# Performance work log

Hardware: AMD Instinct MI355X
Metric: run time of the kernel (lower is better)

The kernel has to match this reference:

```python
import jax, jax.numpy as jnp
import numpy as np

NUM_LAYERS = 2
IN_DIM = 256
OUT_DIM = 256
N = 8192


def setup_inputs() -> dict:
    key = jax.random.key(0)
    k = jax.random.split(key, 7)
    x = jax.random.normal(k[0], (N, IN_DIM), dtype=jnp.float32)
    adj = jax.random.uniform(k[1], (N, N), dtype=jnp.float32)
    # MLP params (Linear: y = x @ W.T + b); kaiming-ish scale
    W1 = jax.random.normal(k[2], (OUT_DIM, IN_DIM), dtype=jnp.float32) / np.sqrt(IN_DIM)
    b1 = jnp.zeros((OUT_DIM,), dtype=jnp.float32)
    W2 = jax.random.normal(k[3], (OUT_DIM, OUT_DIM), dtype=jnp.float32) / np.sqrt(OUT_DIM)
    b2 = jnp.zeros((OUT_DIM,), dtype=jnp.float32)
    epsilon = jnp.zeros((1,), dtype=jnp.float32)  # torch init: Tensor([0.0])
    return {"x": x, "adj": adj, "W1": W1, "b1": b1, "W2": W2, "b2": b2, "epsilon": epsilon}


def reference(x, adj, W1, b1, W2, b2, epsilon):
    for _ in range(NUM_LAYERS):
        # epsilon-weighted neighborhood aggregation + residual
        x = x + epsilon * (adj @ x)          # [N, d]
        # 2-layer MLP (shared across layers, as in the torch module)
        h = jax.nn.relu(x @ W1.T + b1)       # [N, out]
        x = h @ W2.T + b2                    # [N, out]
    return x
```

## Files before the change

### kernel.cpp

```cpp
#include <hip/hip_runtime.h>
#include <hip/hip_bf16.h>

typedef __hip_bfloat16 bf16;
typedef short s16x8 __attribute__((ext_vector_type(8)));
typedef float f32x4 __attribute__((ext_vector_type(4)));

static constexpr int NROWS = 8192;
static constexpr int DIM   = 256;

__device__ inline float to_f(float v) { return v; }
__device__ inline float to_f(bf16 v)  { return __bfloat162float(v); }
__device__ inline unsigned short f2bf(float f) {
    bf16 h = __float2bfloat16(f);
    return __builtin_bit_cast(unsigned short, h);
}

__global__ void convW_kernel(const float* __restrict__ W1, const float* __restrict__ W2,
                             bf16* __restrict__ W1b, bf16* __restrict__ W2b) {
    const int b = blockIdx.x;
    const float* src = (b < 64) ? W1 : W2;
    bf16*       dst = (b < 64) ? W1b : W2b;
    const int t = (b & 63) * 256 + threadIdx.x;
    float4 v = ((const float4*)src)[t];
    ((ushort4*)dst)[t] = make_ushort4(f2bf(v.x), f2bf(v.y), f2bf(v.z), f2bf(v.w));
}

template<typename TIN, bool OUTF32>
__global__ __launch_bounds__(256, 1)
void fused_mlp(const TIN* __restrict__ A, const float* __restrict__ adj,
               const float* __restrict__ eps_p,
               const bf16* __restrict__ W1, const float* __restrict__ b1,
               const bf16* __restrict__ W2, const float* __restrict__ b2,
               void* __restrict__ C) {
    constexpr int K = 256;
    constexpr int PITCH = 264;
    __shared__ short Xs[32][PITCH];
    __shared__ short Hs[32][PITCH];

    const int tid  = threadIdx.x;
    const int lane = tid & 63;
    const int wave = tid >> 6;
    const int lr = lane & 15;
    const int q  = lane >> 4;
    const int row0 = blockIdx.x * 32;
    const float eps = *eps_p;

    if (eps == 0.0f) {
#pragma unroll
        for (int p = 0; p < 4; ++p) {
            const int id = p * 256 + tid;
            const int r  = id >> 5;
            const int c  = (id & 31) * 8;
            if constexpr (sizeof(TIN) == 4) {
                const float* src = (const float*)A + (size_t)(row0 + r) * K + c;
                float4 v0 = *(const float4*)(src);
                float4 v1 = *(const float4*)(src + 4);
                *(ushort4*)(&Xs[r][c])     = make_ushort4(f2bf(v0.x), f2bf(v0.y), f2bf(v0.z), f2bf(v0.w));
                *(ushort4*)(&Xs[r][c + 4]) = make_ushort4(f2bf(v1.x), f2bf(v1.y), f2bf(v1.z), f2bf(v1.w));
            } else {
                *(uint4*)(&Xs[r][c]) = *(const uint4*)((const bf16*)A + (size_t)(row0 + r) * K + c);
            }
        }
    } else {
        for (int r = 0; r < 32; ++r) {
            const int row = row0 + r;
            float s = 0.0f;
            const float* arow = adj + (size_t)row * NROWS;
            for (int k = 0; k < NROWS; ++k)
                s += arow[k] * to_f(A[(size_t)k * DIM + tid]);
            Xs[r][tid] = (short)f2bf(to_f(A[(size_t)row * DIM + tid]) + eps * s);
        }
    }
    __syncthreads();

    f32x4 acc1[4][2] = {};
    const bf16* W1p = W1 + (size_t)(wave * 64 + lr) * K + q * 8;
#pragma unroll
    for (int kk = 0; kk < 8; ++kk) {
        s16x8 wf[4], xf[2];
#pragma unroll
        for (int i = 0; i < 4; ++i)
            wf[i] = *(const s16x8*)(W1p + (size_t)i * 16 * K + kk * 32);
#pragma unroll
        for (int j = 0; j < 2; ++j)
            xf[j] = *(const s16x8*)(&Xs[j * 16 + lr][kk * 32 + q * 8]);
#pragma unroll
        for (int i = 0; i < 4; ++i)
#pragma unroll
            for (int j = 0; j < 2; ++j)
                acc1[i][j] = __builtin_amdgcn_mfma_f32_16x16x32_bf16(
                    wf[i], xf[j], acc1[i][j], 0, 0, 0);
    }

#pragma unroll
    for (int i = 0; i < 4; ++i) {
        const int hc = wave * 64 + i * 16 + q * 4;
        const float4 bv = *(const float4*)(b1 + hc);
#pragma unroll
        for (int j = 0; j < 2; ++j) {
            ushort4 hv;
            hv.x = f2bf(fmaxf(acc1[i][j][0] + bv.x, 0.0f));
            hv.y = f2bf(fmaxf(acc1[i][j][1] + bv.y, 0.0f));
            hv.z = f2bf(fmaxf(acc1[i][j][2] + bv.z, 0.0f));
            hv.w = f2bf(fmaxf(acc1[i][j][3] + bv.w, 0.0f));
            *(ushort4*)(&Hs[j * 16 + lr][hc]) = hv;
        }
    }
    __syncthreads();

    f32x4 acc2[2][4] = {};
    const bf16* W2p = W2 + (size_t)(wave * 64 + lr) * K + q * 8;
#pragma unroll
    for (int kk = 0; kk < 8; ++kk) {
        s16x8 hf[2], wf[4];
#pragma unroll
        for (int j = 0; j < 4; ++j)
            wf[j] = *(const s16x8*)(W2p + (size_t)j * 16 * K + kk * 32);
#pragma unroll
        for (int i = 0; i < 2; ++i)
            hf[i] = *(const s16x8*)(&Hs[i * 16 + lr][kk * 32 + q * 8]);
#pragma unroll
        for (int i = 0; i < 2; ++i)
#pragma unroll
            for (int j = 0; j < 4; ++j)
                acc2[i][j] = __builtin_amdgcn_mfma_f32_16x16x32_bf16(
                    hf[i], wf[j], acc2[i][j], 0, 0, 0);
    }

#pragma unroll
    for (int i = 0; i < 2; ++i) {
#pragma unroll
        for (int j = 0; j < 4; ++j) {
            const int col = wave * 64 + j * 16 + lr;
            const float bv = b2[col];
#pragma unroll
            for (int r = 0; r < 4; ++r) {
                const int row = row0 + i * 16 + q * 4 + r;
                float v = acc2[i][j][r] + bv;
                if (OUTF32) ((float*)C)[(size_t)row * DIM + col] = v;
                else        ((bf16*)C)[(size_t)row * DIM + col] = __float2bfloat16(v);
            }
        }
    }
}

extern "C" void kernel_launch(void* const* d_in, const int* in_sizes, int n_in,
                              void* d_out, int out_size, void* d_ws, size_t ws_size,
                              hipStream_t stream) {
    const float* x   = (const float*)d_in[0];
    const float* adj = (const float*)d_in[1];
    const float* W1  = (const float*)d_in[2];
    const float* b1  = (const float*)d_in[3];
    const float* W2  = (const float*)d_in[4];
    const float* b2  = (const float*)d_in[5];
    const float* eps = (const float*)d_in[6];
    float* out = (float*)d_out;

    char* ws = (char*)d_ws;
    bf16* W1b   = (bf16*)ws;  ws += (size_t)DIM * DIM * 2;
    bf16* W2b   = (bf16*)ws;  ws += (size_t)DIM * DIM * 2;
    bf16* bufY1 = (bf16*)ws;  ws += (size_t)NROWS * DIM * 2;

    convW_kernel<<<128, 256, 0, stream>>>(W1, W2, W1b, W2b);
    fused_mlp<float, false><<<NROWS / 32, 256, 0, stream>>>(x, adj, eps, W1b, b1, W2b, b2, bufY1);
    fused_mlp<bf16,  true ><<<NROWS / 32, 256, 0, stream>>>(bufY1, adj, eps, W1b, b1, W2b, b2, out);
}
```

Measured before the change: 331.9 us.

## Fuse both GIN layers into one kernel with register-resident weight fragments

When epsilon is zero, the two MLP layers now run in a single kernel. The intermediate activations stay in LDS instead of going out to a bf16 global buffer, which removes a kernel launch and a full global round trip. W1 and W2 fragments are loaded into registers once per block and reused across all four GEMM phases, and the output stores are widened to float4. The nonzero-epsilon path moves to separate fallback kernels that exit early, so the default path still pays for two extra empty launches and carries more register pressure from holding 64 weight fragments per thread.

```diff
diff --git a/kernel.cpp b/kernel.cpp
--- a/kernel.cpp
+++ b/kernel.cpp
@@ -7,6 +7,8 @@
 
 static constexpr int NROWS = 8192;
 static constexpr int DIM   = 256;
+static constexpr int KDIM  = 256;
+static constexpr int PITCH = 264;
 
 __device__ inline float to_f(float v) { return v; }
 __device__ inline float to_f(bf16 v)  { return __bfloat162float(v); }
@@ -15,25 +17,133 @@
     return __builtin_bit_cast(unsigned short, h);
 }
 
-__global__ void convW_kernel(const float* __restrict__ W1, const float* __restrict__ W2,
-                             bf16* __restrict__ W1b, bf16* __restrict__ W2b) {
-    const int b = blockIdx.x;
-    const float* src = (b < 64) ? W1 : W2;
-    bf16*       dst = (b < 64) ? W1b : W2b;
-    const int t = (b & 63) * 256 + threadIdx.x;
-    float4 v = ((const float4*)src)[t];
-    ((ushort4*)dst)[t] = make_ushort4(f2bf(v.x), f2bf(v.y), f2bf(v.z), f2bf(v.w));
-}
-
-template<typename TIN, bool OUTF32>
+__global__ void agg0_convW_kernel(const float* __restrict__ x, const float* __restrict__ adj,
+                                  const float* __restrict__ W1, const float* __restrict__ W2,
+                                  const float* __restrict__ eps_p,
+                                  bf16* __restrict__ W1b, bf16* __restrict__ W2b,
+                                  float* __restrict__ y) {
+    {
+        const int b = blockIdx.x;
+        const float* src = (b < 64) ? W1 : W2;
+        bf16*       dst = (b < 64) ? W1b : W2b;
+        const int t = (b & 63) * 256 + threadIdx.x;
+        float4 v = ((const float4*)src)[t];
+        ((ushort4*)dst)[t] = make_ushort4(f2bf(v.x), f2bf(v.y), f2bf(v.z), f2bf(v.w));
+    }
+    const float eps = *eps_p;
+    if (eps == 0.0f) return;
+    const size_t total = (size_t)NROWS * DIM;
+    for (size_t e = (size_t)blockIdx.x * blockDim.x + threadIdx.x;
+         e < total;
+         e += (size_t)gridDim.x * blockDim.x) {
+        const int i = (int)(e >> 8);
+        const int j = (int)(e & 255);
+        float s = 0.0f;
+        const float* arow = adj + (size_t)i * NROWS;
+        for (int k = 0; k < NROWS; ++k)
+            s += arow[k] * x[(size_t)k * DIM + j];
+        y[e] = x[e] + eps * s;
+    }
+}
+
+template<bool RELU>
+__device__ __forceinline__ void mlp_phase_lds(const s16x8 (&wf)[8][4],
+                                              short (*src)[PITCH], short (*dst)[PITCH],
+                                              const float* __restrict__ bias,
+                                              int wave, int lr, int q) {
+    f32x4 acc[4][2] = {};
+#pragma unroll
+    for (int kk = 0; kk < 8; ++kk) {
+        s16x8 xf[2];
+#pragma unroll
+        for (int j = 0; j < 2; ++j)
+            xf[j] = *(const s16x8*)(&src[j * 16 + lr][kk * 32 + q * 8]);
+#pragma unroll
+        for (int i = 0; i < 4; ++i)
+#pragma unroll
+            for (int j = 0; j < 2; ++j)
+                acc[i][j] = __builtin_amdgcn_mfma_f32_16x16x32_bf16(
+                    wf[kk][i], xf[j], acc[i][j], 0, 0, 0);
+    }
+#pragma unroll
+    for (int i = 0; i < 4; ++i) {
+        const int oc = wave * 64 + i * 16 + q * 4;
+        const float4 bv = *(const float4*)(bias + oc);
+#pragma unroll
+        for (int j = 0; j < 2; ++j) {
+            float v0 = acc[i][j][0] + bv.x;
+            float v1 = acc[i][j][1] + bv.y;
+            float v2 = acc[i][j][2] + bv.z;
+            float v3 = acc[i][j][3] + bv.w;
+            if (RELU) {
+                v0 = fmaxf(v0, 0.0f); v1 = fmaxf(v1, 0.0f);
+                v2 = fmaxf(v2, 0.0f); v3 = fmaxf(v3, 0.0f);
+            }
+            *(ushort4*)(&dst[j * 16 + lr][oc]) =
+                make_ushort4(f2bf(v0), f2bf(v1), f2bf(v2), f2bf(v3));
+        }
+    }
+}
+
+template<bool OUTF32>
+__device__ __forceinline__ void mlp_phase_out(const s16x8 (&wf)[8][4],
+                                              short (*src)[PITCH],
+                                              const float* __restrict__ bias,
+                                              void* __restrict__ C,
+                                              int wave, int lr, int q, int row0) {
+    f32x4 acc[4][2] = {};
+#pragma unroll
+    for (int kk = 0; kk < 8; ++kk) {
+        s16x8 xf[2];
+#pragma unroll
+        for (int j = 0; j < 2; ++j)
+            xf[j] = *(const s16x8*)(&src[j * 16 + lr][kk * 32 + q * 8]);
+#pragma unroll
+        for (int i = 0; i < 4; ++i)
+#pragma unroll
+            for (int j = 0; j < 2; ++j)
+                acc[i][j] = __builtin_amdgcn_mfma_f32_16x16x32_bf16(
+                    wf[kk][i], xf[j], acc[i][j], 0, 0, 0);
+    }
+#pragma unroll
+    for (int i = 0; i < 4; ++i) {
+        const int oc = wave * 64 + i * 16 + q * 4;
+        const float4 bv = *(const float4*)(bias + oc);
+#pragma unroll
+        for (int j = 0; j < 2; ++j) {
+            const int row = row0 + j * 16 + lr;
+            float v0 = acc[i][j][0] + bv.x;
+            float v1 = acc[i][j][1] + bv.y;
+            float v2 = acc[i][j][2] + bv.z;
+            float v3 = acc[i][j][3] + bv.w;
+            if (OUTF32) {
+                float4 o; o.x = v0; o.y = v1; o.z = v2; o.w = v3;
+                *(float4*)(&((float*)C)[(size_t)row * DIM + oc]) = o;
+            } else {
+                *(ushort4*)(&((bf16*)C)[(size_t)row * DIM + oc]) =
+                    make_ushort4(f2bf(v0), f2bf(v1), f2bf(v2), f2bf(v3));
+            }
+        }
+    }
+}
+
+__device__ __forceinline__ void load_wfrags(const bf16* __restrict__ W,
+                                            s16x8 (&wf)[8][4],
+                                            int wave, int lr, int q) {
+    const bf16* Wp = W + (size_t)(wave * 64 + lr) * KDIM + q * 8;
+#pragma unroll
+    for (int kk = 0; kk < 8; ++kk)
+#pragma unroll
+        for (int i = 0; i < 4; ++i)
+            wf[kk][i] = *(const s16x8*)(Wp + (size_t)i * 16 * KDIM + kk * 32);
+}
+
 __global__ __launch_bounds__(256, 1)
-void fused_mlp(const TIN* __restrict__ A, const float* __restrict__ adj,
-               const float* __restrict__ eps_p,
-               const bf16* __restrict__ W1, const float* __restrict__ b1,
-               const bf16* __restrict__ W2, const float* __restrict__ b2,
-               void* __restrict__ C) {
-    constexpr int K = 256;
-    constexpr int PITCH = 264;
+void mega_gin(const float* __restrict__ x, const float* __restrict__ eps_p,
+              const bf16* __restrict__ W1, const float* __restrict__ b1,
+              const bf16* __restrict__ W2, const float* __restrict__ b2,
+              float* __restrict__ out) {
+    if (*eps_p != 0.0f) return;
     __shared__ short Xs[32][PITCH];
     __shared__ short Hs[32][PITCH];
 
@@ -43,25 +153,57 @@
     const int lr = lane & 15;
     const int q  = lane >> 4;
     const int row0 = blockIdx.x * 32;
+
+    s16x8 w1f[8][4], w2f[8][4];
+    load_wfrags(W1, w1f, wave, lr, q);
+    load_wfrags(W2, w2f, wave, lr, q);
+
+#pragma unroll
+    for (int p = 0; p < 4; ++p) {
+        const int id = p * 256 + tid;
+        const int r  = id >> 5;
+        const int c  = (id & 31) * 8;
+        const float* src = x + (size_t)(row0 + r) * KDIM + c;
+        float4 v0 = *(const float4*)(src);
+        float4 v1 = *(const float4*)(src + 4);
+        *(ushort4*)(&Xs[r][c])     = make_ushort4(f2bf(v0.x), f2bf(v0.y), f2bf(v0.z), f2bf(v0.w));
+        *(ushort4*)(&Xs[r][c + 4]) = make_ushort4(f2bf(v1.x), f2bf(v1.y), f2bf(v1.z), f2bf(v1.w));
+    }
+    __syncthreads();
+
+    mlp_phase_lds<true >(w1f, Xs, Hs, b1, wave, lr, q);
+    __syncthreads();
+    mlp_phase_lds<false>(w2f, Hs, Xs, b2, wave, lr, q);
+    __syncthreads();
+    mlp_phase_lds<true >(w1f, Xs, Hs, b1, wave, lr, q);
+    __syncthreads();
+    mlp_phase_out<true >(w2f, Hs, b2, out, wave, lr, q, row0);
+}
+
+template<typename TIN, bool OUTF32, bool DO_AGG>
+__global__ __launch_bounds__(256, 1)
+void fb_mlp(const TIN* __restrict__ A, const float* __restrict__ adj,
+            const float* __restrict__ eps_p,
+            const bf16* __restrict__ W1, const float* __restrict__ b1,
+            const bf16* __restrict__ W2, const float* __restrict__ b2,
+            void* __restrict__ C) {
     const float eps = *eps_p;
-
-    if (eps == 0.0f) {
-#pragma unroll
-        for (int p = 0; p < 4; ++p) {
-            const int id = p * 256 + tid;
-            const int r  = id >> 5;
-            const int c  = (id & 31) * 8;
-            if constexpr (sizeof(TIN) == 4) {
-                const float* src = (const float*)A + (size_t)(row0 + r) * K + c;
-                float4 v0 = *(const float4*)(src);
-                float4 v1 = *(const float4*)(src + 4);
-                *(ushort4*)(&Xs[r][c])     = make_ushort4(f2bf(v0.x), f2bf(v0.y), f2bf(v0.z), f2bf(v0.w));
-                *(ushort4*)(&Xs[r][c + 4]) = make_ushort4(f2bf(v1.x), f2bf(v1.y), f2bf(v1.z), f2bf(v1.w));
-            } else {
-                *(uint4*)(&Xs[r][c]) = *(const uint4*)((const bf16*)A + (size_t)(row0 + r) * K + c);
-            }
-        }
-    } else {
+    if (eps == 0.0f) return;
+    __shared__ short Xs[32][PITCH];
+    __shared__ short Hs[32][PITCH];
+
+    const int tid  = threadIdx.x;
+    const int lane = tid & 63;
+    const int wave = tid >> 6;
+    const int lr = lane & 15;
+    const int q  = lane >> 4;
+    const int row0 = blockIdx.x * 32;
+
+    s16x8 w1f[8][4], w2f[8][4];
+    load_wfrags(W1, w1f, wave, lr, q);
+    load_wfrags(W2, w2f, wave, lr, q);
+
+    if (DO_AGG) {
         for (int r = 0; r < 32; ++r) {
             const int row = row0 + r;
             float s = 0.0f;
@@ -70,78 +212,28 @@
                 s += arow[k] * to_f(A[(size_t)k * DIM + tid]);
             Xs[r][tid] = (short)f2bf(to_f(A[(size_t)row * DIM + tid]) + eps * s);
         }
-    }
-    __syncthreads();
-
-    f32x4 acc1[4][2] = {};
-    const bf16* W1p = W1 + (size_t)(wave * 64 + lr) * K + q * 8;
-#pragma unroll
-    for (int kk = 0; kk < 8; ++kk) {
-        s16x8 wf[4], xf[2];
-#pragma unroll
-        for (int i = 0; i < 4; ++i)
-            wf[i] = *(const s16x8*)(W1p + (size_t)i * 16 * K + kk * 32);
-#pragma unroll
-        for (int j = 0; j < 2; ++j)
-            xf[j] = *(const s16x8*)(&Xs[j * 16 + lr][kk * 32 + q * 8]);
-#pragma unroll
-        for (int i = 0; i < 4; ++i)
-#pragma unroll
-            for (int j = 0; j < 2; ++j)
-                acc1[i][j] = __builtin_amdgcn_mfma_f32_16x16x32_bf16(
-                    wf[i], xf[j], acc1[i][j], 0, 0, 0);
-    }
-
-#pragma unroll
-    for (int i = 0; i < 4; ++i) {
-        const int hc = wave * 64 + i * 16 + q * 4;
-        const float4 bv = *(const float4*)(b1 + hc);
-#pragma unroll
-        for (int j = 0; j < 2; ++j) {
-            ushort4 hv;
-            hv.x = f2bf(fmaxf(acc1[i][j][0] + bv.x, 0.0f));
-            hv.y = f2bf(fmaxf(acc1[i][j][1] + bv.y, 0.0f));
-            hv.z = f2bf(fmaxf(acc1[i][j][2] + bv.z, 0.0f));
-            hv.w = f2bf(fmaxf(acc1[i][j][3] + bv.w, 0.0f));
-            *(ushort4*)(&Hs[j * 16 + lr][hc]) = hv;
-        }
-    }
-    __syncthreads();
-
-    f32x4 acc2[2][4] = {};
-    const bf16* W2p = W2 + (size_t)(wave * 64 + lr) * K + q * 8;
-#pragma unroll
-    for (int kk = 0; kk < 8; ++kk) {
-        s16x8 hf[2], wf[4];
-#pragma unroll
-        for (int j = 0; j < 4; ++j)
-            wf[j] = *(const s16x8*)(W2p + (size_t)j * 16 * K + kk * 32);
-#pragma unroll
-        for (int i = 0; i < 2; ++i)
-            hf[i] = *(const s16x8*)(&Hs[i * 16 + lr][kk * 32 + q * 8]);
-#pragma unroll
-        for (int i = 0; i < 2; ++i)
-#pragma unroll
-            for (int j = 0; j < 4; ++j)
-                acc2[i][j] = __builtin_amdgcn_mfma_f32_16x16x32_bf16(
-                    hf[i], wf[j], acc2[i][j], 0, 0, 0);
-    }
-
-#pragma unroll
-    for (int i = 0; i < 2; ++i) {
-#pragma unroll
-        for (int j = 0; j < 4; ++j) {
-            const int col = wave * 64 + j * 16 + lr;
-            const float bv = b2[col];
-#pragma unroll
-            for (int r = 0; r < 4; ++r) {
-                const int row = row0 + i * 16 + q * 4 + r;
-                float v = acc2[i][j][r] + bv;
-                if (OUTF32) ((float*)C)[(size_t)row * DIM + col] = v;
-                else        ((bf16*)C)[(size_t)row * DIM + col] = __float2bfloat16(v);
+    } else {
+#pragma unroll
+        for (int p = 0; p < 4; ++p) {
+            const int id = p * 256 + tid;
+            const int r  = id >> 5;
+            const int c  = (id & 31) * 8;
+            if constexpr (sizeof(TIN) == 4) {
+                const float* src = (const float*)A + (size_t)(row0 + r) * KDIM + c;
+                float4 v0 = *(const float4*)(src);
+                float4 v1 = *(const float4*)(src + 4);
+                *(ushort4*)(&Xs[r][c])     = make_ushort4(f2bf(v0.x), f2bf(v0.y), f2bf(v0.z), f2bf(v0.w));
+                *(ushort4*)(&Xs[r][c + 4]) = make_ushort4(f2bf(v1.x), f2bf(v1.y), f2bf(v1.z), f2bf(v1.w));
+            } else {
+                *(uint4*)(&Xs[r][c]) = *(const uint4*)((const bf16*)A + (size_t)(row0 + r) * KDIM + c);
             }
         }
     }
+    __syncthreads();
+
+    mlp_phase_lds<true >(w1f, Xs, Hs, b1, wave, lr, q);
+    __syncthreads();
+    mlp_phase_out<OUTF32>(w2f, Hs, b2, C, wave, lr, q, row0);
 }
 
 extern "C" void kernel_launch(void* const* d_in, const int* in_sizes, int n_in,
@@ -157,11 +249,13 @@
     float* out = (float*)d_out;
 
     char* ws = (char*)d_ws;
-    bf16* W1b   = (bf16*)ws;  ws += (size_t)DIM * DIM * 2;
-    bf16* W2b   = (bf16*)ws;  ws += (size_t)DIM * DIM * 2;
-    bf16* bufY1 = (bf16*)ws;  ws += (size_t)NROWS * DIM * 2;
-
-    convW_kernel<<<128, 256, 0, stream>>>(W1, W2, W1b, W2b);
-    fused_mlp<float, false><<<NROWS / 32, 256, 0, stream>>>(x, adj, eps, W1b, b1, W2b, b2, bufY1);
-    fused_mlp<bf16,  true ><<<NROWS / 32, 256, 0, stream>>>(bufY1, adj, eps, W1b, b1, W2b, b2, out);
-}
+    bf16*  W1b  = (bf16*)ws;  ws += (size_t)DIM * DIM * 2;
+    bf16*  W2b  = (bf16*)ws;  ws += (size_t)DIM * DIM * 2;
+    float* agg0 = (float*)ws; ws += (size_t)NROWS * DIM * 4;
+    bf16*  mid  = (bf16*)ws;  ws += (size_t)NROWS * DIM * 2;
+
+    agg0_convW_kernel<<<128, 256, 0, stream>>>(x, adj, W1, W2, eps, W1b, W2b, agg0);
+    mega_gin<<<NROWS / 32, 256, 0, stream>>>(x, eps, W1b, b1, W2b, b2, out);
+    fb_mlp<float, false, false><<<NROWS / 32, 256, 0, stream>>>(agg0, adj, eps, W1b, b1, W2b, b2, mid);
+    fb_mlp<bf16,  true,  true ><<<NROWS / 32, 256, 0, stream>>>(mid,  adj, eps, W1b, b1, W2b, b2, out);
+}
```

After: 328.2 us. No clear change (-1.1%).
